# Kernel tuning notes

Hardware: AMD Instinct MI355X
Metric: run time of the kernel (lower is better)

The kernel has to match this reference:

```python
import jax, jax.numpy as jnp
import numpy as np

Q_HEADS, KV_HEADS, HEAD_SIZE, H, MAX_LEN = 16, 4, 64, 1024, 4096
B, S = 1, 4096


def _rope_tables(max_len, head_size):
    half = head_size // 2
    inv_freq = 1.0 / (10000.0 ** (np.arange(half, dtype=np.float32) / half))
    pos = np.arange(max_len, dtype=np.float32)
    ang = pos[:, None] * inv_freq[None, :]  # [max_len, half]
    return jnp.asarray(np.sin(ang)), jnp.asarray(np.cos(ang))


def setup_inputs() -> dict:
    key = jax.random.key(0)
    ks = jax.random.split(key, 6)
    sc = 1.0 / np.sqrt(H)
    x = jax.random.normal(ks[0], (B, S, H), dtype=jnp.float32)
    wq = jax.random.normal(ks[1], (H, H), dtype=jnp.float32) * sc
    wk = jax.random.normal(ks[2], (H, KV_HEADS * HEAD_SIZE), dtype=jnp.float32) * sc
    wv = jax.random.normal(ks[3], (H, KV_HEADS * HEAD_SIZE), dtype=jnp.float32) * sc
    wo = jax.random.normal(ks[4], (H, H), dtype=jnp.float32) * sc
    sin, cos = _rope_tables(MAX_LEN, HEAD_SIZE)
    full_mask = jnp.tril(jnp.ones((MAX_LEN, MAX_LEN), dtype=bool))
    attention_mask = jnp.ones((B, S), dtype=jnp.int32)
    return {"x": x, "attention_mask": attention_mask, "start": 0,
            "wq": wq, "wk": wk, "wv": wv, "wo": wo,
            "sin": sin, "cos": cos, "full_mask": full_mask}


def _rotate(t, sin, cos, start):
    # t: [b, heads, s, head_size]; interleaved even/odd RoPE
    s = t.shape[2]
    sn = sin[start:start + s, :][None, None, :, :]
    cs = cos[start:start + s, :][None, None, :, :]
    even, odd = t[..., 0::2], t[..., 1::2]
    out_even = cs * even - sn * odd
    out_odd = sn * even + cs * odd
    return jnp.stack((out_even, out_odd), axis=-1).reshape(t.shape)


def _expand_kv(t, group):
    # [b, kv_heads, s, d] -> [b, kv_heads*group, s, d]
    b, kvh, s, d = t.shape
    return jnp.broadcast_to(t[:, :, None], (b, kvh, group, s, d)).reshape(b, kvh * group, s, d)


def reference(x, attention_mask, start, wq, wk, wv, wo, sin, cos, full_mask):
    b, s, _ = x.shape
    group = Q_HEADS // KV_HEADS
    Q = (x @ wq).reshape(b, s, Q_HEADS, HEAD_SIZE).transpose(0, 2, 1, 3)
    K = (x @ wk).reshape(b, s, KV_HEADS, HEAD_SIZE).transpose(0, 2, 1, 3)
    V = (x @ wv).reshape(b, s, KV_HEADS, HEAD_SIZE).transpose(0, 2, 1, 3)
    Q = _rotate(Q, sin, cos, start)
    K = _rotate(K, sin, cos, start)
    K = _expand_kv(K, group)
    V = _expand_kv(V, group)
    z = jnp.einsum('bhqd,bhkd->bhqk', Q, K) / (HEAD_SIZE ** 0.5)
    kv_len = start + s
    mask = full_mask[:s, :kv_len][None, None, :, :]
    amask = (attention_mask[:, :kv_len] != 0)[:, None, None, :]
    mask = mask & amask
    z = jnp.where(mask, z, -1000000.0)
    A = jax.nn.softmax(z, axis=-1)
    ctx = jnp.einsum('bhqk,bhkd->bhqd', A, V)
    q_mask = attention_mask[:, :s].astype(ctx.dtype)[:, None, :, None]
    ctx = ctx * q_mask
    ctx = ctx.transpose(0, 2, 1, 3).reshape(b, s, H)
    return ctx @ wo
```

## Files before the change

kernel.cpp:

```cpp
#include <hip/hip_runtime.h>

typedef __bf16 bf16x8 __attribute__((ext_vector_type(8)));
typedef float f32x4 __attribute__((ext_vector_type(4)));
typedef unsigned int u32x4 __attribute__((ext_vector_type(4)));

typedef const void __attribute__((address_space(1)))* gas1;
typedef void __attribute__((address_space(3)))* las3;

__device__ __forceinline__ unsigned short f2bf(float f) {
  unsigned int u = __builtin_bit_cast(unsigned int, f);
  u += 0x7fffu + ((u >> 16) & 1u);
  return (unsigned short)(u >> 16);
}
__device__ __forceinline__ float bf2f(unsigned short h) {
  unsigned int u = ((unsigned int)h) << 16;
  return __builtin_bit_cast(float, u);
}
__device__ __forceinline__ unsigned int pack2bf(float lo, float hi) {
  return (unsigned int)f2bf(lo) | ((unsigned int)f2bf(hi) << 16);
}
__device__ __forceinline__ unsigned int packtr(float lo, float hi) {
  return __builtin_amdgcn_perm(__builtin_bit_cast(unsigned int, hi),
                               __builtin_bit_cast(unsigned int, lo), 0x07060302u);
}

__global__ __launch_bounds__(256) void prep(const float* __restrict__ x,
                                            const float* __restrict__ wq,
                                            const float* __restrict__ wk,
                                            const float* __restrict__ wv,
                                            const float* __restrict__ wo,
                                            const float* __restrict__ sinT,
                                            const float* __restrict__ cosT,
                                            unsigned short* __restrict__ xb,
                                            unsigned short* __restrict__ wtqkv,
                                            unsigned short* __restrict__ wot,
                                            float2* __restrict__ scT) {
  __shared__ float tile[32][33];
  const int b = blockIdx.x;
  const int tid = threadIdx.x;
  if (b < 4096) {
    int i = b * 256 + tid;
    float4 v = ((const float4*)x)[i];
    uint2 o;
    o.x = pack2bf(v.x, v.y);
    o.y = pack2bf(v.z, v.w);
    ((uint2*)xb)[i] = o;
    return;
  }
  if (b >= 6656) {
    int idx = (b - 6656) * 256 + tid;
    scT[idx] = make_float2(sinT[idx], cosT[idx]);
    return;
  }
  const float* src;
  unsigned short* dst;
  int R, C, t;
  if (b < 5120)      { t = b - 4096; src = wq; dst = wtqkv;               R = 1024; C = 1024; }
  else if (b < 5376) { t = b - 5120; src = wk; dst = wtqkv + 1024 * 1024; R = 1024; C = 256; }
  else if (b < 5632) { t = b - 5376; src = wv; dst = wtqkv + 1280 * 1024; R = 1024; C = 256; }
  else               { t = b - 5632; src = wo; dst = wot;                 R = 1024; C = 1024; }
  const int ntc = C >> 5;
  const int c0 = (t % ntc) * 32, r0 = (t / ntc) * 32;
  const int tx = tid & 31, ty = tid >> 5;
#pragma unroll
  for (int i = 0; i < 4; ++i)
    tile[ty + i * 8][tx] = src[(r0 + ty + i * 8) * C + c0 + tx];
  __syncthreads();
#pragma unroll
  for (int i = 0; i < 4; ++i)
    dst[(c0 + ty + i * 8) * R + r0 + tx] = f2bf(tile[tx][ty + i * 8]);
}


__device__ __forceinline__ void stage_tile(const unsigned short* __restrict__ src,
                                           unsigned short* lds, int tid) {
  const int w = tid >> 6;
  const int l = tid & 63;
  const int rsub = l >> 3;
  const int cblk = l & 7;
#pragma unroll
  for (int i = 0; i < 4; ++i) {
    const int row = i * 32 + w * 8 + rsub;
    const int scol = (cblk ^ (row & 7)) * 8;
    __builtin_amdgcn_global_load_lds((gas1)(const void*)&src[(size_t)row * 1024 + scol],
                                     (las3)(void*)&lds[(i * 32 + w * 8) * 64], 16, 0, 0);
  }
}

#define GEMM_STEP(CUR, NXT, KNEXT, DO_STAGE)                                          \
  {                                                                                   \
    if (DO_STAGE) {                                                                   \
      stage_tile(Ab + (KNEXT), sm[NXT][0], tid);                                      \
      stage_tile(Bb + (KNEXT), sm[NXT][1], tid);                                      \
    }                                                                                 \
    const char* As = (const char*)sm[CUR][0];                                         \
    const char* Bs = (const char*)sm[CUR][1];                                         \
    bf16x8 af[2][4], bfr[2][4];                                                       \
    _Pragma("unroll")                                                                 \
    for (int kk = 0; kk < 2; ++kk) {                                                  \
      const int co = (kk * 64 + lgrp * 16) ^ xorsel;                                  \
      _Pragma("unroll")                                                               \
      for (int mi = 0; mi < 4; ++mi)                                                  \
        af[kk][mi] = __builtin_bit_cast(bf16x8,                                       \
            *(const u32x4*)(As + arow + mi * 2048 + co));                             \
      _Pragma("unroll")                                                               \
      for (int ni = 0; ni < 4; ++ni)                                                  \
        bfr[kk][ni] = __builtin_bit_cast(bf16x8,                                      \
            *(const u32x4*)(Bs + brow + ni * 2048 + co));                             \
    }                                                                                 \
    _Pragma("unroll")                                                                 \
    for (int kk = 0; kk < 2; ++kk)                                                    \
      _Pragma("unroll")                                                               \
      for (int mi = 0; mi < 4; ++mi)                                                  \
        _Pragma("unroll")                                                             \
        for (int ni = 0; ni < 4; ++ni)                                                \
          acc[mi][ni] = __builtin_amdgcn_mfma_f32_16x16x32_bf16(af[kk][mi],           \
                            bfr[kk][ni], acc[mi][ni], 0, 0, 0);                       \
    __syncthreads();                                                                  \
  }

__global__ __launch_bounds__(256, 2) void gemm_qkv(const unsigned short* __restrict__ A,
                                                   const unsigned short* __restrict__ Bt,
                                                   const float2* __restrict__ scT,
                                                   unsigned short* __restrict__ Qh,
                                                   unsigned short* __restrict__ Kh,
                                                   unsigned short* __restrict__ Vt) {
  __shared__ __align__(16) unsigned short sm[2][2][128 * 64];
  const int tid = threadIdx.x;
  const int bid = blockIdx.x;
  const int swz = (bid & 7) * 48 + (bid >> 3);
  const int nt = swz % 12, mt = swz / 12;
  const int m0 = mt * 128, n0 = nt * 128;

  const int lane = tid & 63, wid = tid >> 6;
  const int wr = wid >> 1, wc = wid & 1;
  const int lgrp = lane >> 4, lmod = lane & 15;
  const int xorsel = (lmod & 7) << 4;
  const int arow = (wr * 64 + lmod) * 128;
  const int brow = (wc * 64 + lmod) * 128;

  const unsigned short* Ab = A + (size_t)m0 * 1024;
  const unsigned short* Bb = Bt + (size_t)n0 * 1024;

  f32x4 acc[4][4] = {};

  stage_tile(Ab, sm[0][0], tid);
  stage_tile(Bb, sm[0][1], tid);
  __syncthreads();

  for (int t = 0; t < 16; t += 2) {
    GEMM_STEP(0, 1, (size_t)(t + 1) * 64, true);
    GEMM_STEP(1, 0, (size_t)(t + 2) * 64, t < 14);
  }

  const int ncol0 = n0 + wc * 64;
  if (ncol0 >= 1280) {
    const int kvh = (ncol0 - 1280) >> 6;
#pragma unroll
    for (int mi = 0; mi < 4; ++mi)
#pragma unroll
      for (int ni = 0; ni < 4; ++ni) {
        int d = ni * 16 + lmod;
        int s = m0 + wr * 64 + mi * 16 + lgrp * 4;
        uint2 o;
        o.x = pack2bf(acc[mi][ni][0], acc[mi][ni][1]);
        o.y = pack2bf(acc[mi][ni][2], acc[mi][ni][3]);
        *(uint2*)&Vt[((size_t)(kvh * 64 + d)) * 4096 + s] = o;
      }
    return;
  }

  const float qscale = 0.18033688011112042f;
  const bool isQ = (ncol0 < 1024);
  const int h = isQ ? (ncol0 >> 6) : ((ncol0 - 1024) >> 6);
  unsigned short* dstbase = isQ ? Qh : Kh;
  const bool evn = (lmod & 1) == 0;
#pragma unroll
  for (int mi = 0; mi < 4; ++mi)
#pragma unroll
    for (int ni = 0; ni < 4; ++ni) {
      int d = ni * 16 + lmod;
      int i = d >> 1;
#pragma unroll
      for (int r = 0; r < 4; ++r) {
        float v = acc[mi][ni][r];
        float pp = __shfl_xor(v, 1, 64);
        int row = m0 + wr * 64 + mi * 16 + lgrp * 4 + r;
        float2 sc = scT[(size_t)row * 32 + i];
        float e = evn ? v : pp, o = evn ? pp : v;
        float outv = evn ? (sc.y * e - sc.x * o) : (sc.x * e + sc.y * o);
        if (isQ) outv *= qscale;
        dstbase[((size_t)h * 4096 + row) * 64 + d] = f2bf(outv);
      }
    }
}

__global__ __launch_bounds__(256, 2) void gemm_out(const unsigned short* __restrict__ A,
                                                   const unsigned short* __restrict__ Bt,
                                                   float* __restrict__ Cout) {
  __shared__ __align__(16) unsigned short sm[2][2][128 * 64];
  const int tid = threadIdx.x;
  const int bid = blockIdx.x;
  const int swz = (bid & 7) * 32 + (bid >> 3);
  const int nt = swz & 7, mt = swz >> 3;
  const int m0 = mt * 128, n0 = nt * 128;

  const int lane = tid & 63, wid = tid >> 6;
  const int wr = wid >> 1, wc = wid & 1;
  const int lgrp = lane >> 4, lmod = lane & 15;
  const int xorsel = (lmod & 7) << 4;
  const int arow = (wr * 64 + lmod) * 128;
  const int brow = (wc * 64 + lmod) * 128;

  const unsigned short* Ab = A + (size_t)m0 * 1024;
  const unsigned short* Bb = Bt + (size_t)n0 * 1024;

  f32x4 acc[4][4] = {};

  stage_tile(Ab, sm[0][0], tid);
  stage_tile(Bb, sm[0][1], tid);
  __syncthreads();

  for (int t = 0; t < 16; t += 2) {
    GEMM_STEP(0, 1, (size_t)(t + 1) * 64, true);
    GEMM_STEP(1, 0, (size_t)(t + 2) * 64, t < 14);
  }

#pragma unroll
  for (int mi = 0; mi < 4; ++mi)
#pragma unroll
    for (int ni = 0; ni < 4; ++ni)
#pragma unroll
      for (int r = 0; r < 4; ++r) {
        int row = m0 + wr * 64 + mi * 16 + lgrp * 4 + r;
        int col = n0 + wc * 64 + ni * 16 + lmod;
        Cout[(size_t)row * 1024 + col] = acc[mi][ni][r];
      }
}

__global__ __launch_bounds__(256, 4) void attn4(const unsigned short* __restrict__ Qh,
                                                const unsigned short* __restrict__ Kh,
                                                const unsigned short* __restrict__ Vt,
                                                unsigned short* __restrict__ ctx) {
  __shared__ __align__(16) unsigned short Kls[128 * 68];
  __shared__ __align__(16) unsigned short Vls[64 * 136];
  const int bx = blockIdx.x;
  const int head = bx & 15;
  const int qidx = bx >> 4;
  const int qh = (qidx < 32) ? (63 - qidx) : (qidx - 32);
  const int kvh = head >> 2;
  const int tid = threadIdx.x;
  const int wave = tid >> 6, lane = tid & 63;
  const int lgrp = lane >> 4, lmod = lane & 15;
  const int qbase = qh * 64;
  const int ntile = qh >> 1;

  const unsigned short* Kg = Kh + (size_t)kvh * 4096 * 64;
  const unsigned short* Vg = Vt + (size_t)kvh * 64 * 4096;

  const int qrow = qbase + wave * 16 + lmod;
  const unsigned short* Qg = Qh + ((size_t)head * 4096 + qrow) * 64;
  bf16x8 qf0 = __builtin_bit_cast(bf16x8, *(const u32x4*)&Qg[lgrp * 8]);
  bf16x8 qf1 = __builtin_bit_cast(bf16x8, *(const u32x4*)&Qg[32 + lgrp * 8]);

  const int kbase = (8 * (lmod >> 2) + (lmod & 3)) * 68 + lgrp * 8;
  const int vbase = lmod * 136 + lgrp * 8;

  f32x4 accO[4] = {};
  float m_i = -3e38f, l_i = 0.f;

  for (int kc = 0; kc <= ntile; ++kc) {
    const int kb = kc * 128;
    __syncthreads();
#pragma unroll
    for (int i = 0; i < 4; ++i) {
      int ii = tid + i * 256;
      int r = ii >> 3, sg = (ii & 7) * 8;
      u32x4 dK = *(const u32x4*)&Kg[(size_t)(kb + r) * 64 + sg];
      uint2* pd = (uint2*)&Kls[r * 68 + sg];
      pd[0] = make_uint2(dK[0], dK[1]);
      pd[1] = make_uint2(dK[2], dK[3]);
    }
#pragma unroll
    for (int i = 0; i < 4; ++i) {
      int ii = tid + i * 256;
      int r = ii >> 4, sg = (ii & 15) * 8;
      *(u32x4*)&Vls[r * 136 + sg] = *(const u32x4*)&Vg[(size_t)r * 4096 + kb + sg];
    }
    __syncthreads();

    f32x4 s[4][2];
    __builtin_amdgcn_s_setprio(1);
#pragma unroll
    for (int g = 0; g < 4; ++g)
#pragma unroll
      for (int t = 0; t < 2; ++t) {
        const unsigned short* ka = &Kls[kbase + (32 * g + 4 * t) * 68];
        uint2 a0 = *(const uint2*)&ka[0];
        uint2 a1 = *(const uint2*)&ka[4];
        uint2 b0 = *(const uint2*)&ka[32];
        uint2 b1 = *(const uint2*)&ka[36];
        u32x4 lo = {a0.x, a0.y, a1.x, a1.y};
        u32x4 hi = {b0.x, b0.y, b1.x, b1.y};
        bf16x8 alo = __builtin_bit_cast(bf16x8, lo);
        bf16x8 ahi = __builtin_bit_cast(bf16x8, hi);
        f32x4 z = {};
        z = __builtin_amdgcn_mfma_f32_16x16x32_bf16(alo, qf0, z, 0, 0, 0);
        z = __builtin_amdgcn_mfma_f32_16x16x32_bf16(ahi, qf1, z, 0, 0, 0);
        s[g][t] = z;
      }
    __builtin_amdgcn_s_setprio(0);

    if (kb + 127 > qbase + wave * 16) {
#pragma unroll
      for (int g = 0; g < 4; ++g)
#pragma unroll
        for (int t = 0; t < 2; ++t)
#pragma unroll
          for (int r = 0; r < 4; ++r) {
            int key = kb + 32 * g + 8 * lgrp + 4 * t + r;
            if (key > qrow) s[g][t][r] = -3e38f;
          }
    }

    {
      f32x4 v0 = s[0][0], v1 = s[0][1];
#pragma unroll
      for (int g = 1; g < 4; ++g)
#pragma unroll
        for (int r = 0; r < 4; ++r) {
          v0[r] = fmaxf(v0[r], s[g][0][r]);
          v1[r] = fmaxf(v1[r], s[g][1][r]);
        }
      float mx = fmaxf(fmaxf(fmaxf(v0[0], v0[1]), fmaxf(v0[2], v0[3])),
                       fmaxf(fmaxf(v1[0], v1[1]), fmaxf(v1[2], v1[3])));
      mx = fmaxf(mx, __shfl_xor(mx, 16, 64));
      mx = fmaxf(mx, __shfl_xor(mx, 32, 64));
      float mnew = fmaxf(m_i, mx);
      float alpha = __builtin_amdgcn_exp2f(m_i - mnew);
      m_i = mnew;
      f32x4 su = {};
#pragma unroll
      for (int g = 0; g < 4; ++g)
#pragma unroll
        for (int t = 0; t < 2; ++t)
#pragma unroll
          for (int r = 0; r < 4; ++r) {
            float ev = __builtin_amdgcn_exp2f(s[g][t][r] - mnew);
            s[g][t][r] = ev;
            su[r] += ev;
          }
      float rs = (su[0] + su[1]) + (su[2] + su[3]);
      rs += __shfl_xor(rs, 16, 64);
      rs += __shfl_xor(rs, 32, 64);
      l_i = l_i * alpha + rs;
#pragma unroll
      for (int dt = 0; dt < 4; ++dt)
#pragma unroll
        for (int r = 0; r < 4; ++r) accO[dt][r] *= alpha;
    }

    __builtin_amdgcn_s_setprio(1);
#pragma unroll
    for (int g = 0; g < 4; ++g) {
      u32x4 pk;
      pk[0] = packtr(s[g][0][0], s[g][0][1]);
      pk[1] = packtr(s[g][0][2], s[g][0][3]);
      pk[2] = packtr(s[g][1][0], s[g][1][1]);
      pk[3] = packtr(s[g][1][2], s[g][1][3]);
      bf16x8 pf = __builtin_bit_cast(bf16x8, pk);
#pragma unroll
      for (int dt = 0; dt < 4; ++dt) {
        bf16x8 vf = __builtin_bit_cast(bf16x8, *(const u32x4*)&Vls[vbase + dt * 2176 + 32 * g]);
        accO[dt] = __builtin_amdgcn_mfma_f32_16x16x32_bf16(vf, pf, accO[dt], 0, 0, 0);
      }
    }
    __builtin_amdgcn_s_setprio(0);
  }

  {
    float inv = 1.f / l_i;
#pragma unroll
    for (int dt = 0; dt < 4; ++dt) {
      uint2 o;
      o.x = pack2bf(accO[dt][0] * inv, accO[dt][1] * inv);
      o.y = pack2bf(accO[dt][2] * inv, accO[dt][3] * inv);
      *(uint2*)&ctx[(size_t)qrow * 1024 + head * 64 + dt * 16 + lgrp * 4] = o;
    }
  }
}

extern "C" void kernel_launch(void* const* d_in, const int* in_sizes, int n_in,
                              void* d_out, int out_size, void* d_ws, size_t ws_size,
                              hipStream_t stream) {
  const float* x    = (const float*)d_in[0];
  const float* wq   = (const float*)d_in[3];
  const float* wk   = (const float*)d_in[4];
  const float* wv   = (const float*)d_in[5];
  const float* wo   = (const float*)d_in[6];
  const float* sinT = (const float*)d_in[7];
  const float* cosT = (const float*)d_in[8];

  unsigned short* ws    = (unsigned short*)d_ws;
  unsigned short* xb    = ws;
  unsigned short* wtqkv = xb + 4096 * 1024;
  unsigned short* wot   = wtqkv + 1536 * 1024;
  unsigned short* Qh    = wot + 1024 * 1024;
  unsigned short* Kh    = Qh + 16 * 4096 * 64;
  unsigned short* Vt    = Kh + 4 * 4096 * 64;
  unsigned short* ctx   = Vt + 4 * 64 * 4096;
  float2* scT           = (float2*)(ctx + 4096 * 1024);
  float* out = (float*)d_out;

  prep<<<7168, 256, 0, stream>>>(x, wq, wk, wv, wo, sinT, cosT, xb, wtqkv, wot, scT);
  gemm_qkv<<<384, 256, 0, stream>>>(xb, wtqkv, scT, Qh, Kh, Vt);
  attn4<<<dim3(1024), 256, 0, stream>>>(Qh, Kh, Vt, ctx);
  gemm_out<<<256, 256, 0, stream>>>(ctx, wot, out);
}
```

Before: 232.6 us.

## Load V fragments directly from global into registers in attention kernel

Removes the shared-memory staging of V tiles in the attention kernel; each lane now loads its V fragments straight from global memory into registers, double-buffered across the four key groups and interleaved with the PV MFMAs. This cuts LDS traffic and LDS footprint, which may allow more occupancy, and removes the cooperative V copy before the barrier. The cost is that each of the four waves independently re-reads the same V data from global/L2 instead of sharing one copy, and the latency of those loads now falls inside the compute loop.

```diff
diff --git a/kernel.cpp b/kernel.cpp
--- a/kernel.cpp
+++ b/kernel.cpp
@@ -238,12 +238,11 @@
       }
 }
 
-__global__ __launch_bounds__(256, 4) void attn4(const unsigned short* __restrict__ Qh,
+__global__ __launch_bounds__(256, 4) void attn5(const unsigned short* __restrict__ Qh,
                                                 const unsigned short* __restrict__ Kh,
                                                 const unsigned short* __restrict__ Vt,
                                                 unsigned short* __restrict__ ctx) {
   __shared__ __align__(16) unsigned short Kls[128 * 68];
-  __shared__ __align__(16) unsigned short Vls[64 * 136];
   const int bx = blockIdx.x;
   const int head = bx & 15;
   const int qidx = bx >> 4;
@@ -257,6 +256,7 @@
 
   const unsigned short* Kg = Kh + (size_t)kvh * 4096 * 64;
   const unsigned short* Vg = Vt + (size_t)kvh * 64 * 4096;
+  const unsigned short* Vbase = Vg + (size_t)lmod * 4096 + lgrp * 8;
 
   const int qrow = qbase + wave * 16 + lmod;
   const unsigned short* Qg = Qh + ((size_t)head * 4096 + qrow) * 64;
@@ -264,7 +264,6 @@
   bf16x8 qf1 = __builtin_bit_cast(bf16x8, *(const u32x4*)&Qg[32 + lgrp * 8]);
 
   const int kbase = (8 * (lmod >> 2) + (lmod & 3)) * 68 + lgrp * 8;
-  const int vbase = lmod * 136 + lgrp * 8;
 
   f32x4 accO[4] = {};
   float m_i = -3e38f, l_i = 0.f;
@@ -280,12 +279,6 @@
       uint2* pd = (uint2*)&Kls[r * 68 + sg];
       pd[0] = make_uint2(dK[0], dK[1]);
       pd[1] = make_uint2(dK[2], dK[3]);
-    }
-#pragma unroll
-    for (int i = 0; i < 4; ++i) {
-      int ii = tid + i * 256;
-      int r = ii >> 4, sg = (ii & 15) * 8;
-      *(u32x4*)&Vls[r * 136 + sg] = *(const u32x4*)&Vg[(size_t)r * 4096 + kb + sg];
     }
     __syncthreads();
 
@@ -311,6 +304,11 @@
       }
     __builtin_amdgcn_s_setprio(0);
 
+    u32x4 vA[4], vB[4];
+#pragma unroll
+    for (int dt = 0; dt < 4; ++dt)
+      vA[dt] = *(const u32x4*)&Vbase[(size_t)dt * 65536 + kb];
+
     if (kb + 127 > qbase + wave * 16) {
 #pragma unroll
       for (int g = 0; g < 4; ++g)
@@ -360,22 +358,45 @@
         for (int r = 0; r < 4; ++r) accO[dt][r] *= alpha;
     }
 
+#define PACK_P(g, pf)                                                      \
+    {                                                                      \
+      u32x4 pk;                                                            \
+      pk[0] = packtr(s[g][0][0], s[g][0][1]);                              \
+      pk[1] = packtr(s[g][0][2], s[g][0][3]);                              \
+      pk[2] = packtr(s[g][1][0], s[g][1][1]);                              \
+      pk[3] = packtr(s[g][1][2], s[g][1][3]);                              \
+      pf = __builtin_bit_cast(bf16x8, pk);                                 \
+    }
+#define PV_G(vregs, pf)                                                    \
+    _Pragma("unroll")                                                      \
+    for (int dt = 0; dt < 4; ++dt) {                                       \
+      bf16x8 vf = __builtin_bit_cast(bf16x8, vregs[dt]);                   \
+      accO[dt] = __builtin_amdgcn_mfma_f32_16x16x32_bf16(vf, pf, accO[dt], 0, 0, 0); \
+    }
+
+    bf16x8 pf0, pf1, pf2, pf3;
+    PACK_P(0, pf0);
+    PACK_P(1, pf1);
+    PACK_P(2, pf2);
+    PACK_P(3, pf3);
+
+#pragma unroll
+    for (int dt = 0; dt < 4; ++dt)
+      vB[dt] = *(const u32x4*)&Vbase[(size_t)dt * 65536 + kb + 32];
     __builtin_amdgcn_s_setprio(1);
-#pragma unroll
-    for (int g = 0; g < 4; ++g) {
-      u32x4 pk;
-      pk[0] = packtr(s[g][0][0], s[g][0][1]);
-      pk[1] = packtr(s[g][0][2], s[g][0][3]);
-      pk[2] = packtr(s[g][1][0], s[g][1][1]);
-      pk[3] = packtr(s[g][1][2], s[g][1][3]);
-      bf16x8 pf = __builtin_bit_cast(bf16x8, pk);
-#pragma unroll
-      for (int dt = 0; dt < 4; ++dt) {
-        bf16x8 vf = __builtin_bit_cast(bf16x8, *(const u32x4*)&Vls[vbase + dt * 2176 + 32 * g]);
-        accO[dt] = __builtin_amdgcn_mfma_f32_16x16x32_bf16(vf, pf, accO[dt], 0, 0, 0);
-      }
-    }
+    PV_G(vA, pf0);
+#pragma unroll
+    for (int dt = 0; dt < 4; ++dt)
+      vA[dt] = *(const u32x4*)&Vbase[(size_t)dt * 65536 + kb + 64];
+    PV_G(vB, pf1);
+#pragma unroll
+    for (int dt = 0; dt < 4; ++dt)
+      vB[dt] = *(const u32x4*)&Vbase[(size_t)dt * 65536 + kb + 96];
+    PV_G(vA, pf2);
+    PV_G(vB, pf3);
     __builtin_amdgcn_s_setprio(0);
+#undef PACK_P
+#undef PV_G
   }
 
   {
@@ -414,6 +435,6 @@
 
   prep<<<7168, 256, 0, stream>>>(x, wq, wk, wv, wo, sinT, cosT, xb, wtqkv, wot, scT);
   gemm_qkv<<<384, 256, 0, stream>>>(xb, wtqkv, scT, Qh, Kh, Vt);
-  attn4<<<dim3(1024), 256, 0, stream>>>(Qh, Kh, Vt, ctx);
+  attn5<<<dim3(1024), 256, 0, stream>>>(Qh, Kh, Vt, ctx);
   gemm_out<<<256, 256, 0, stream>>>(ctx, wot, out);
 }
```

Result: slower. 307.2 us (+32.1%).

## Load attention K/V tiles directly to LDS with XOR-swizzled layout

Applied to the files above, without the earlier changes.

The attention kernel now fills its K and V shared-memory tiles with direct global-to-LDS loads instead of staging them through registers, and drops the padded layouts in favour of an XOR-swizzled layout meant to avoid bank conflicts. K fragments are read as single 16-byte LDS loads using a remapped key order, and the causal mask index and P packing are changed to match. The aim is to cut register traffic and LDS store instructions during tile loading. The cost is extra index arithmetic, and correctness depends on the key permutation being consistent across the QK, mask and PV steps.

```diff
diff --git a/kernel.cpp b/kernel.cpp
--- a/kernel.cpp
+++ b/kernel.cpp
@@ -238,12 +238,12 @@
       }
 }
 
-__global__ __launch_bounds__(256, 4) void attn4(const unsigned short* __restrict__ Qh,
+__global__ __launch_bounds__(256, 4) void attn6(const unsigned short* __restrict__ Qh,
                                                 const unsigned short* __restrict__ Kh,
                                                 const unsigned short* __restrict__ Vt,
                                                 unsigned short* __restrict__ ctx) {
-  __shared__ __align__(16) unsigned short Kls[128 * 68];
-  __shared__ __align__(16) unsigned short Vls[64 * 136];
+  __shared__ __align__(16) unsigned short Kls[128 * 64];
+  __shared__ __align__(16) unsigned short Vls[64 * 128];
   const int bx = blockIdx.x;
   const int head = bx & 15;
   const int qidx = bx >> 4;
@@ -263,9 +263,6 @@
   bf16x8 qf0 = __builtin_bit_cast(bf16x8, *(const u32x4*)&Qg[lgrp * 8]);
   bf16x8 qf1 = __builtin_bit_cast(bf16x8, *(const u32x4*)&Qg[32 + lgrp * 8]);
 
-  const int kbase = (8 * (lmod >> 2) + (lmod & 3)) * 68 + lgrp * 8;
-  const int vbase = lmod * 136 + lgrp * 8;
-
   f32x4 accO[4] = {};
   float m_i = -3e38f, l_i = 0.f;
 
@@ -275,17 +272,18 @@
 #pragma unroll
     for (int i = 0; i < 4; ++i) {
       int ii = tid + i * 256;
-      int r = ii >> 3, sg = (ii & 7) * 8;
-      u32x4 dK = *(const u32x4*)&Kg[(size_t)(kb + r) * 64 + sg];
-      uint2* pd = (uint2*)&Kls[r * 68 + sg];
-      pd[0] = make_uint2(dK[0], dK[1]);
-      pd[1] = make_uint2(dK[2], dK[3]);
+      int r = ii >> 3, b = ii & 7;
+      __builtin_amdgcn_global_load_lds(
+          (gas1)(const void*)&Kg[(size_t)(kb + r) * 64 + ((b ^ (r & 7)) * 8)],
+          (las3)(void*)&Kls[(size_t)ii * 8], 16, 0, 0);
     }
 #pragma unroll
     for (int i = 0; i < 4; ++i) {
       int ii = tid + i * 256;
-      int r = ii >> 4, sg = (ii & 15) * 8;
-      *(u32x4*)&Vls[r * 136 + sg] = *(const u32x4*)&Vg[(size_t)r * 4096 + kb + sg];
+      int d = ii >> 4, b = ii & 15;
+      __builtin_amdgcn_global_load_lds(
+          (gas1)(const void*)&Vg[(size_t)d * 4096 + kb + ((b ^ (d & 15)) * 8)],
+          (las3)(void*)&Vls[(size_t)ii * 8], 16, 0, 0);
     }
     __syncthreads();
 
@@ -295,15 +293,11 @@
     for (int g = 0; g < 4; ++g)
 #pragma unroll
       for (int t = 0; t < 2; ++t) {
-        const unsigned short* ka = &Kls[kbase + (32 * g + 4 * t) * 68];
-        uint2 a0 = *(const uint2*)&ka[0];
-        uint2 a1 = *(const uint2*)&ka[4];
-        uint2 b0 = *(const uint2*)&ka[32];
-        uint2 b1 = *(const uint2*)&ka[36];
-        u32x4 lo = {a0.x, a0.y, a1.x, a1.y};
-        u32x4 hi = {b0.x, b0.y, b1.x, b1.y};
-        bf16x8 alo = __builtin_bit_cast(bf16x8, lo);
-        bf16x8 ahi = __builtin_bit_cast(bf16x8, hi);
+        const int row = 32 * g + t + 2 * lmod;
+        bf16x8 alo = __builtin_bit_cast(bf16x8,
+            *(const u32x4*)&Kls[(size_t)row * 64 + ((lgrp ^ (row & 7)) * 8)]);
+        bf16x8 ahi = __builtin_bit_cast(bf16x8,
+            *(const u32x4*)&Kls[(size_t)row * 64 + (((4 + lgrp) ^ (row & 7)) * 8)]);
         f32x4 z = {};
         z = __builtin_amdgcn_mfma_f32_16x16x32_bf16(alo, qf0, z, 0, 0, 0);
         z = __builtin_amdgcn_mfma_f32_16x16x32_bf16(ahi, qf1, z, 0, 0, 0);
@@ -318,7 +312,7 @@
         for (int t = 0; t < 2; ++t)
 #pragma unroll
           for (int r = 0; r < 4; ++r) {
-            int key = kb + 32 * g + 8 * lgrp + 4 * t + r;
+            int key = kb + 32 * g + 8 * lgrp + 2 * r + t;
             if (key > qrow) s[g][t][r] = -3e38f;
           }
     }
@@ -364,14 +358,16 @@
 #pragma unroll
     for (int g = 0; g < 4; ++g) {
       u32x4 pk;
-      pk[0] = packtr(s[g][0][0], s[g][0][1]);
-      pk[1] = packtr(s[g][0][2], s[g][0][3]);
-      pk[2] = packtr(s[g][1][0], s[g][1][1]);
-      pk[3] = packtr(s[g][1][2], s[g][1][3]);
+      pk[0] = packtr(s[g][0][0], s[g][1][0]);
+      pk[1] = packtr(s[g][0][1], s[g][1][1]);
+      pk[2] = packtr(s[g][0][2], s[g][1][2]);
+      pk[3] = packtr(s[g][0][3], s[g][1][3]);
       bf16x8 pf = __builtin_bit_cast(bf16x8, pk);
 #pragma unroll
       for (int dt = 0; dt < 4; ++dt) {
-        bf16x8 vf = __builtin_bit_cast(bf16x8, *(const u32x4*)&Vls[vbase + dt * 2176 + 32 * g]);
+        const int d = dt * 16 + lmod;
+        bf16x8 vf = __builtin_bit_cast(bf16x8,
+            *(const u32x4*)&Vls[(size_t)d * 128 + (((4 * g + lgrp) ^ lmod) * 8)]);
         accO[dt] = __builtin_amdgcn_mfma_f32_16x16x32_bf16(vf, pf, accO[dt], 0, 0, 0);
       }
     }
@@ -414,6 +410,6 @@
 
   prep<<<7168, 256, 0, stream>>>(x, wq, wk, wv, wo, sinT, cosT, xb, wtqkv, wot, scT);
   gemm_qkv<<<384, 256, 0, stream>>>(xb, wtqkv, scT, Qh, Kh, Vt);
-  attn4<<<dim3(1024), 256, 0, stream>>>(Qh, Kh, Vt, ctx);
+  attn6<<<dim3(1024), 256, 0, stream>>>(Qh, Kh, Vt, ctx);
   gemm_out<<<256, 256, 0, stream>>>(ctx, wot, out);
 }
```

New measurement: 216.2 us. 7.0% less time.
